# Optimization experiments

Hardware: AMD Instinct MI355X
Metric: run time of the kernel (lower is better)

## Reference

```python
import jax, jax.numpy as jnp
import numpy as np

PRED_LEN = 24
F, I, H = 64, 128, 512  # features_size, input_size, hidden_size
B, S = 1024, 168        # batch, seq_len


def setup_inputs() -> dict:
    key = jax.random.key(0)
    ks = jax.random.split(key, 14)
    s = 0.05
    return {
        "x": jax.random.normal(ks[0], (B, S, F), dtype=jnp.float32),
        "W_enc": jax.random.normal(ks[1], (I, F), dtype=jnp.float32) * s,
        "b_enc": jax.random.normal(ks[2], (I,), dtype=jnp.float32) * s,
        "Wih0": jax.random.normal(ks[3], (4 * H, I), dtype=jnp.float32) * s,
        "Whh0": jax.random.normal(ks[4], (4 * H, H), dtype=jnp.float32) * s,
        "bih0": jax.random.normal(ks[5], (4 * H,), dtype=jnp.float32) * s,
        "bhh0": jax.random.normal(ks[6], (4 * H,), dtype=jnp.float32) * s,
        "Wih1": jax.random.normal(ks[7], (4 * H, H), dtype=jnp.float32) * s,
        "Whh1": jax.random.normal(ks[8], (4 * H, H), dtype=jnp.float32) * s,
        "bih1": jax.random.normal(ks[9], (4 * H,), dtype=jnp.float32) * s,
        "bhh1": jax.random.normal(ks[10], (4 * H,), dtype=jnp.float32) * s,
        "W_dec": jax.random.normal(ks[11], (F, H), dtype=jnp.float32) * s,
        "b_dec": jax.random.normal(ks[12], (F,), dtype=jnp.float32) * s,
    }


def _lstm_cell(xt, h, c, Wih, Whh, bih, bhh):
    # PyTorch gate order: i, f, g, o
    gates = xt @ Wih.T + h @ Whh.T + (bih + bhh)
    i, f, g, o = jnp.split(gates, 4, axis=-1)
    c = jax.nn.sigmoid(f) * c + jax.nn.sigmoid(i) * jnp.tanh(g)
    h = jax.nn.sigmoid(o) * jnp.tanh(c)
    return h, c


def reference(x, W_enc, b_enc, Wih0, Whh0, bih0, bhh0,
              Wih1, Whh1, bih1, bhh1, W_dec, b_dec):
    batch = x.shape[0]
    h0 = jnp.zeros((batch, H), x.dtype)
    init = (h0, h0, h0, h0)  # (h_l0, c_l0, h_l1, c_l1)

    def step(carry, xt):
        hl0, cl0, hl1, cl1 = carry
        enc = xt @ W_enc.T + b_enc
        hl0, cl0 = _lstm_cell(enc, hl0, cl0, Wih0, Whh0, bih0, bhh0)
        hl1, cl1 = _lstm_cell(hl0, hl1, cl1, Wih1, Whh1, bih1, bhh1)
        out = hl1 @ W_dec.T + b_dec
        return (hl0, cl0, hl1, cl1), out

    # teacher-forced pass over the observed sequence; keep only last output
    carry, outs = jax.lax.scan(step, init, jnp.transpose(x, (1, 0, 2)))
    last = outs[-1]  # [B, F], prediction for step seq_len (idx = seq_len-1)

    def ar_step(state, _):
        carry, prev = state
        carry, out = step(carry, prev)
        return (carry, out), out

    _, ar_outs = jax.lax.scan(ar_step, (carry, last), None, length=PRED_LEN - 1)
    outputs = jnp.concatenate([last[None], ar_outs], axis=0)  # [pred_len, B, F]
    return jnp.transpose(outputs, (1, 0, 2))  # [B, pred_len, F]
```

## Files before the change

### kernel.cpp

```cpp
#include <hip/hip_runtime.h>

#define B_   1024
#define S_   168
#define F_   64
#define I_   128
#define H_   512
#define G4   2048
#define PRED 24

typedef unsigned short u16;
typedef unsigned int   u32;
typedef __attribute__((ext_vector_type(8))) __bf16 bf16x8;
typedef __attribute__((ext_vector_type(4))) float  f32x4;
typedef __attribute__((ext_vector_type(4))) int    i32x4;

__device__ __forceinline__ u16 f2bf(float f) {
  u32 u = __float_as_uint(f);
  u += 0x7fff + ((u >> 16) & 1);
  return (u16)(u >> 16);
}
__device__ __forceinline__ float bf2f(u16 h) {
  return __uint_as_float(((u32)h) << 16);
}
__device__ __forceinline__ float sigm(float x) {
  x = fminf(fmaxf(x, -30.f), 30.f);
  return 1.f / (1.f + __expf(-x));
}
__device__ __forceinline__ float tanh_(float x) {
  x = fminf(fmaxf(x, -15.f), 15.f);
  float e = __expf(2.f * x);
  return (e - 1.f) / (e + 1.f);
}


__global__ void k_split(const float* __restrict__ src, u16* __restrict__ hi,
                        u16* __restrict__ lo, int n) {
  for (int i = blockIdx.x * 256 + threadIdx.x; i < n; i += gridDim.x * 256) {
    float a = src[i];
    u16 h = f2bf(a);
    hi[i] = h;
    lo[i] = f2bf(a - bf2f(h));
  }
}

__global__ void k_w0c(const float* __restrict__ Wih0, const float* __restrict__ Wenc,
                      float* __restrict__ W0c) {
  int id = blockIdx.x * 256 + threadIdx.x;
  int j = id >> 6, f = id & 63;
  float s = 0.f;
  for (int i = 0; i < 128; ++i) s += Wih0[j * 128 + i] * Wenc[i * 64 + f];
  W0c[id] = s;
}

__global__ void k_w0cd(const float* __restrict__ W0c, const float* __restrict__ Wdec,
                       float* __restrict__ W0cd) {
  int id = blockIdx.x * 256 + threadIdx.x;
  int j = id >> 9, m = id & 511;
  float s = 0.f;
  for (int f = 0; f < 64; ++f) s += W0c[j * 64 + f] * Wdec[f * 512 + m];
  W0cd[id] = s;
}

__global__ void k_biases(const float* __restrict__ Wih0, const float* __restrict__ benc,
                         const float* __restrict__ bih0, const float* __restrict__ bhh0,
                         const float* __restrict__ bih1, const float* __restrict__ bhh1,
                         float* __restrict__ b0c, float* __restrict__ b1c) {
  int j = blockIdx.x * 256 + threadIdx.x;
  float s = 0.f;
  for (int i = 0; i < 128; ++i) s += Wih0[j * 128 + i] * benc[i];
  b0c[j] = s + bih0[j] + bhh0[j];
  b1c[j] = bih1[j] + bhh1[j];
}

__global__ void k_b0ar(const float* __restrict__ W0c, const float* __restrict__ bdec,
                       const float* __restrict__ b0c, float* __restrict__ b0ar) {
  int j = blockIdx.x * 256 + threadIdx.x;
  float s = 0.f;
  for (int f = 0; f < 64; ++f) s += W0c[j * 64 + f] * bdec[f];
  b0ar[j] = b0c[j] + s;
}

__global__ void k_pack(const float* __restrict__ W, int K, u16* __restrict__ dst) {
  int id = blockIdx.x * 256 + threadIdx.x;
  int lane = id & 63, fi = id >> 6;
  int NK = K >> 5;
  int kt = fi % NK, jg = fi / NK;
  int g = jg & 3, jt = jg >> 2;
  int j = jt * 16 + (lane & 15);
  int kb = kt * 32 + (lane >> 4) * 8;
  const float* src = W + (size_t)(g * 512 + j) * K + kb;
  u16 hi[8] __attribute__((aligned(16)));
  u16 lo[8] __attribute__((aligned(16)));
#pragma unroll
  for (int e = 0; e < 8; ++e) {
    float v = src[e];
    u16 h = f2bf(v);
    hi[e] = h;
    lo[e] = f2bf(v - bf2f(h));
  }
  u16* d = dst + (size_t)fi * 1024 + lane * 8;
  *(i32x4*)d = *(const i32x4*)hi;
  *(i32x4*)(d + 512) = *(const i32x4*)lo;
}


struct CellArgs {
  const u16* A1hi; const u16* A1lo; int strideA1; int K1;
  const u16* W1p;
  const u16* A2hi; const u16* A2lo;
  const u16* W2p;
  const float* bias;
  float* c;
  u16* hhi; u16* hlo;
};

struct DecArgs {
  const u16* hhi; const u16* hlo;
  const float* Wdec; const float* bdec;
  float* out;
};

__device__ __forceinline__ void cell_body(const CellArgs& P, u16* smem_,
                                          int t, int jblk, int mblk) {
  const u16* __restrict__ A1hi = P.A1hi;
  const u16* __restrict__ A1lo = P.A1lo;
  const int strideA1 = P.strideA1;
  const int K1 = P.K1;
  const u16* __restrict__ W1p = P.W1p;
  const u16* __restrict__ A2hi = P.A2hi;
  const u16* __restrict__ A2lo = P.A2lo;
  const u16* __restrict__ W2p = P.W2p;
  const float* __restrict__ bias = P.bias;
  float* __restrict__ c = P.c;
  u16* __restrict__ hhi = P.hhi;
  u16* __restrict__ hlo = P.hlo;

  const int mbase = mblk * 64;
  const int lane = t & 63, wv = t >> 6;
  const int mi = wv >> 1, jh = wv & 1;
  const int lr = lane & 15, qk = lane >> 4;
  const int jtg = jblk * 2 + jh;
  const int nc1 = (K1 == 64) ? 1 : 4;
  const int NC  = nc1 + 4;
  const int NK1 = K1 >> 5;

  f32x4 acc[4];
#pragma unroll
  for (int g = 0; g < 4; ++g) acc[g] = (f32x4){0.f, 0.f, 0.f, 0.f};

  auto prm = [&](int cc, const u16*& Ah, const u16*& Al, int& st, int& kb, int& Kc,
                 const u16*& Wp, int& NK) {
    if (cc < nc1) { Ah = A1hi; Al = A1lo; st = strideA1; kb = cc * 128;
                    Kc = (K1 == 64) ? 64 : 128; Wp = W1p; NK = NK1; }
    else { int i = cc - nc1; Ah = A2hi; Al = A2lo; st = 512; kb = i * 128;
           Kc = 128; Wp = W2p; NK = 16; }
  };

  auto stageLoad = [&](int cc, i32x4* rr) {
    const u16 *Ah, *Al, *Wp_; int st, kb, Kc, NK;
    prm(cc, Ah, Al, st, kb, Kc, Wp_, NK);
    const int ppr = Kc >> 3;
    const int npc = (Kc == 128) ? 4 : 2;
#pragma unroll 4
    for (int p = 0; p < npc; ++p) {
      int li   = p * 512 + t;
      int part = li >= 64 * ppr;
      int liw  = li - part * 64 * ppr;
      int rown = (ppr == 16) ? (liw >> 4) : (liw >> 3);
      int kp   = liw & (ppr - 1);
      const u16* src = (part ? Al : Ah) + (size_t)(mbase + rown) * st + kb + kp * 8;
      rr[p] = *(const i32x4*)src;
    }
  };
  auto stageWrite = [&](int cc, const i32x4* rr, int buf) {
    const int Kc  = (cc < nc1 && K1 == 64) ? 64 : 128;
    const int ppr = Kc >> 3;
    const int npc = (Kc == 128) ? 4 : 2;
    u16* sb = smem_ + buf * 16384;
#pragma unroll 4
    for (int p = 0; p < npc; ++p) {
      int li   = p * 512 + t;
      int part = li >= 64 * ppr;
      int liw  = li - part * 64 * ppr;
      int rown = (ppr == 16) ? (liw >> 4) : (liw >> 3);
      int kp   = liw & (ppr - 1);
      *(i32x4*)&sb[(((part * 64 + rown) * ppr) + (kp ^ (rown & (ppr - 1)))) * 8] = rr[p];
    }
  };
  auto loadW = [&](const u16* Wp_, int NK, int kt, i32x4* wh, i32x4* wl) {
#pragma unroll
    for (int g = 0; g < 4; ++g) {
      const u16* p = Wp_ + (size_t)((jtg * 4 + g) * NK + kt) * 1024 + lane * 8;
      wh[g] = *(const i32x4*)p;
      wl[g] = *(const i32x4*)(p + 512);
    }
  };
  auto mstep = [&](int buf, int ppr, const u16* Wp_, int NK, int kb5) {
    const u16* sb = smem_ + buf * 16384;
    const int nkt  = ppr >> 2;
    const int rowA = mi * 16 + lr;
    const int rmask = rowA & (ppr - 1);
#pragma unroll 4
    for (int kt = 0; kt < nkt; ++kt) {
      i32x4 wh[4], wl[4];
      loadW(Wp_, NK, kb5 + kt, wh, wl);
      int pl = (kt * 4 + qk) ^ rmask;
      bf16x8 ah = *(const bf16x8*)&sb[(rowA * ppr + pl) * 8];
      bf16x8 al = *(const bf16x8*)&sb[((64 + rowA) * ppr + pl) * 8];
#pragma unroll
      for (int g = 0; g < 4; ++g) {
        bf16x8 bh = __builtin_bit_cast(bf16x8, wh[g]);
        bf16x8 bl = __builtin_bit_cast(bf16x8, wl[g]);
        acc[g] = __builtin_amdgcn_mfma_f32_16x16x32_bf16(ah, bh, acc[g], 0, 0, 0);
        acc[g] = __builtin_amdgcn_mfma_f32_16x16x32_bf16(al, bh, acc[g], 0, 0, 0);
        acc[g] = __builtin_amdgcn_mfma_f32_16x16x32_bf16(ah, bl, acc[g], 0, 0, 0);
      }
    }
  };

  i32x4 sreg[4];

  stageLoad(0, sreg);
  stageWrite(0, sreg, 0);
  __syncthreads();

  for (int cc = 0; cc < NC; ++cc) {
    const int buf  = cc & 1;
    const bool more = (cc + 1 < NC);
    if (more) stageLoad(cc + 1, sreg);
    {
      const u16 *Ah, *Al, *Wp_; int st, kb, Kc, NK;
      prm(cc, Ah, Al, st, kb, Kc, Wp_, NK);
      mstep(buf, Kc >> 3, Wp_, NK, kb >> 5);
    }
    if (more) stageWrite(cc + 1, sreg, buf ^ 1);
    __syncthreads();
  }

  const int   j   = jblk * 32 + jh * 16 + lr;
  const float bi  = bias[j];
  const float bff = bias[512 + j];
  const float bg  = bias[1024 + j];
  const float bo  = bias[1536 + j];
#pragma unroll
  for (int rr = 0; rr < 4; ++rr) {
    int b   = mbase + mi * 16 + qk * 4 + rr;
    int idx = b * 512 + j;
    float iv = sigm(acc[0][rr] + bi);
    float fv = sigm(acc[1][rr] + bff);
    float gv = tanh_(acc[2][rr] + bg);
    float ov = sigm(acc[3][rr] + bo);
    float cn = fv * c[idx] + iv * gv;
    c[idx] = cn;
    float hn = ov * tanh_(cn);
    u16 hh = f2bf(hn);
    hhi[idx] = hh;
    hlo[idx] = f2bf(hn - bf2f(hh));
  }
}

__device__ __forceinline__ void dec_body(const DecArgs& D, float* smemf,
                                         int t, int bx, int by) {
  if (by >= 8) return;
  float (*sH)[65] = (float (*)[65])smemf;
  const int bbase = bx * 64;
  const int mbase = by * 64;
  {
    int b  = bbase + (t >> 3);
    int m0 = (t & 7) * 8;
    i32x4 hv = *(const i32x4*)&D.hhi[(size_t)b * 512 + mbase + m0];
    i32x4 lv = *(const i32x4*)&D.hlo[(size_t)b * 512 + mbase + m0];
    const u16* hp = (const u16*)&hv;
    const u16* lp = (const u16*)&lv;
#pragma unroll
    for (int e = 0; e < 8; ++e)
      sH[t >> 3][m0 + e] = bf2f(hp[e]) + bf2f(lp[e]);
  }
  __syncthreads();
  const int bl = t & 63;
  const int wv = t >> 6;
  float acc[8];
#pragma unroll
  for (int u = 0; u < 8; ++u) acc[u] = 0.f;
  for (int m = 0; m < 64; ++m) {
    float hv = sH[bl][m];
#pragma unroll
    for (int u = 0; u < 8; ++u)
      acc[u] += hv * D.Wdec[(size_t)(u * 8 + wv) * 512 + mbase + m];
  }
#pragma unroll
  for (int u = 0; u < 8; ++u) {
    int f = u * 8 + wv;
    float v = acc[u];
    if (by == 0) v += D.bdec[f];
    atomicAdd(&D.out[(size_t)(bbase + bl) * (PRED * F_) + f], v);
  }
}


__global__ __launch_bounds__(512, 4) void lstm3(CellArgs a) {
  __shared__ __align__(16) u16 smem_[32768];
  cell_body(a, smem_, threadIdx.x, blockIdx.x, blockIdx.y);
}

__global__ __launch_bounds__(512, 4) void lstm3_dual(CellArgs a0, CellArgs a1) {
  __shared__ __align__(16) u16 smem_[32768];
  if (blockIdx.z == 0) cell_body(a0, smem_, threadIdx.x, blockIdx.x, blockIdx.y);
  else                 cell_body(a1, smem_, threadIdx.x, blockIdx.x, blockIdx.y);
}

__global__ __launch_bounds__(512, 4) void lstm3_cell_dec(CellArgs a, DecArgs d) {
  __shared__ __align__(16) u16 smem_[32768];
  if (blockIdx.z == 0) cell_body(a, smem_, threadIdx.x, blockIdx.x, blockIdx.y);
  else                 dec_body(d, (float*)smem_, threadIdx.x, blockIdx.x, blockIdx.y);
}

__global__ __launch_bounds__(512) void k_decoder2(DecArgs d) {
  __shared__ __align__(16) float sm[64 * 65];
  dec_body(d, sm, threadIdx.x, blockIdx.x, blockIdx.y);
}


extern "C" void kernel_launch(void* const* d_in, const int* in_sizes, int n_in,
                              void* d_out, int out_size, void* d_ws, size_t ws_size,
                              hipStream_t stream) {
  const float* x    = (const float*)d_in[0];
  const float* Wenc = (const float*)d_in[1];
  const float* benc = (const float*)d_in[2];
  const float* Wih0 = (const float*)d_in[3];
  const float* Whh0 = (const float*)d_in[4];
  const float* bih0 = (const float*)d_in[5];
  const float* bhh0 = (const float*)d_in[6];
  const float* Wih1 = (const float*)d_in[7];
  const float* Whh1 = (const float*)d_in[8];
  const float* bih1 = (const float*)d_in[9];
  const float* bhh1 = (const float*)d_in[10];
  const float* Wdec = (const float*)d_in[11];
  const float* bdec = (const float*)d_in[12];
  float* out = (float*)d_out;

  char* p = (char*)d_ws;
  auto carve = [&](size_t bytes) { char* r = p; p += (bytes + 255) & ~(size_t)255; return r; };
  const size_t NX = (size_t)B_ * S_ * F_;
  const size_t NH = (size_t)B_ * H_;
  const size_t WP512 = (size_t)G4 * 512 * 2;
  u16* Xhi    = (u16*)carve(NX * 2);
  u16* Xlo    = (u16*)carve(NX * 2);
  float* W0c  = (float*)carve((size_t)G4 * 64 * 4);
  float* W0cd = (float*)carve((size_t)G4 * 512 * 4);
  u16* W0cp   = (u16*)carve((size_t)G4 * 64 * 2 * 2);
  u16* W0cdp  = (u16*)carve(WP512 * 2);
  u16* Whh0p  = (u16*)carve(WP512 * 2);
  u16* Wih1p  = (u16*)carve(WP512 * 2);
  u16* Whh1p  = (u16*)carve(WP512 * 2);
  float* b0c  = (float*)carve(G4 * 4);
  float* b0ar = (float*)carve(G4 * 4);
  float* b1c  = (float*)carve(G4 * 4);
  u16* h0hi[2] = {(u16*)carve(NH * 2), (u16*)carve(NH * 2)};
  u16* h0lo[2] = {(u16*)carve(NH * 2), (u16*)carve(NH * 2)};
  u16* h1hi[2] = {(u16*)carve(NH * 2), (u16*)carve(NH * 2)};
  u16* h1lo[2] = {(u16*)carve(NH * 2), (u16*)carve(NH * 2)};
  float* c0 = (float*)carve(NH * 4);
  float* c1 = (float*)carve(NH * 4);
  (void)ws_size; (void)n_in; (void)in_sizes;

  hipMemsetAsync(d_out, 0, (size_t)out_size * 4, stream);
  hipMemsetAsync(h0hi[0], 0, NH * 2, stream);
  hipMemsetAsync(h0lo[0], 0, NH * 2, stream);
  hipMemsetAsync(h1hi[0], 0, NH * 2, stream);
  hipMemsetAsync(h1lo[0], 0, NH * 2, stream);
  hipMemsetAsync(c0, 0, NH * 4, stream);
  hipMemsetAsync(c1, 0, NH * 4, stream);

  k_split<<<4096, 256, 0, stream>>>(x, Xhi, Xlo, (int)NX);
  k_w0c<<<512, 256, 0, stream>>>(Wih0, Wenc, W0c);
  k_w0cd<<<4096, 256, 0, stream>>>(W0c, Wdec, W0cd);
  k_biases<<<8, 256, 0, stream>>>(Wih0, benc, bih0, bhh0, bih1, bhh1, b0c, b1c);
  k_b0ar<<<8, 256, 0, stream>>>(W0c, bdec, b0c, b0ar);
  k_pack<<<32 * 16, 256, 0, stream>>>(Whh0, 512, Whh0p);
  k_pack<<<32 * 16, 256, 0, stream>>>(Wih1, 512, Wih1p);
  k_pack<<<32 * 16, 256, 0, stream>>>(Whh1, 512, Whh1p);
  k_pack<<<32 * 16, 256, 0, stream>>>(W0cd, 512, W0cdp);
  k_pack<<<32 * 2, 256, 0, stream>>>(W0c, 64, W0cp);

  dim3 grid(16, 16);
  dim3 grid2(16, 16, 2);

  {
    CellArgs l0 = {Xhi, Xlo, S_ * F_, 64, W0cp,
                   h0hi[0], h0lo[0], Whh0p, b0c, c0, h0hi[1], h0lo[1]};
    lstm3<<<grid, 512, 0, stream>>>(l0);
  }
  for (int s = 0; s < S_ - 1; ++s) {
    int pp = s & 1, np = 1 - pp;
    CellArgs l1 = {h0hi[np], h0lo[np], 512, 512, Wih1p,
                   h1hi[pp], h1lo[pp], Whh1p, b1c, c1, h1hi[np], h1lo[np]};
    CellArgs l0 = {Xhi + (size_t)(s + 1) * F_, Xlo + (size_t)(s + 1) * F_, S_ * F_, 64, W0cp,
                   h0hi[np], h0lo[np], Whh0p, b0c, c0, h0hi[pp], h0lo[pp]};
    lstm3_dual<<<grid2, 512, 0, stream>>>(l1, l0);
  }
  {
    CellArgs l1 = {h0hi[0], h0lo[0], 512, 512, Wih1p,
                   h1hi[1], h1lo[1], Whh1p, b1c, c1, h1hi[0], h1lo[0]};
    lstm3<<<grid, 512, 0, stream>>>(l1);
  }

  for (int s = S_ - 1; s < S_ + PRED - 1; ++s) {
    int pp = s & 1, np = 1 - pp;
    DecArgs d = {h1hi[np], h1lo[np], Wdec, bdec, out + (size_t)(s - (S_ - 1)) * F_};
    if (s + 1 < S_ + PRED - 1) {
      CellArgs l0 = {h1hi[np], h1lo[np], 512, 512, W0cdp,
                     h0hi[np], h0lo[np], Whh0p, b0ar, c0, h0hi[pp], h0lo[pp]};
      lstm3_cell_dec<<<grid2, 512, 0, stream>>>(l0, d);
      CellArgs l1 = {h0hi[pp], h0lo[pp], 512, 512, Wih1p,
                     h1hi[np], h1lo[np], Whh1p, b1c, c1, h1hi[pp], h1lo[pp]};
      lstm3<<<grid, 512, 0, stream>>>(l1);
    } else {
      k_decoder2<<<dim3(16, 8), 512, 0, stream>>>(d);
    }
  }
}
```

Baseline: 8.297 ms.

## Software-pipeline weight fragment loads and remap cell block indices for L2 locality

```diff
diff --git a/kernel.cpp b/kernel.cpp
--- a/kernel.cpp
+++ b/kernel.cpp
@@ -103,6 +103,9 @@
   *(i32x4*)(d + 512) = *(const i32x4*)lo;
 }
 
+
+struct PPR16 { static constexpr int v = 16; };
+struct PPR8  { static constexpr int v = 8;  };
 
 struct CellArgs {
   const u16* A1hi; const u16* A1lo; int strideA1; int K1;
@@ -195,31 +198,47 @@
       wl[g] = *(const i32x4*)(p + 512);
     }
   };
-  auto mstep = [&](int buf, int ppr, const u16* Wp_, int NK, int kb5) {
+
+  i32x4 whA[4], wlA[4];
+
+  auto mstep = [&](auto PPRt, int buf, const u16* WpC, int NKC, int kb5C,
+                   const u16* WpN, int NKN, int kb5N, bool haveNext) {
+    constexpr int ppr = decltype(PPRt)::v;
+    constexpr int nkt = ppr >> 2;
     const u16* sb = smem_ + buf * 16384;
-    const int nkt  = ppr >> 2;
     const int rowA = mi * 16 + lr;
     const int rmask = rowA & (ppr - 1);
-#pragma unroll 4
+#pragma unroll
     for (int kt = 0; kt < nkt; ++kt) {
-      i32x4 wh[4], wl[4];
-      loadW(Wp_, NK, kb5 + kt, wh, wl);
+      i32x4 whN[4], wlN[4];
+      const bool pf = (kt + 1 < nkt) || haveNext;
+      if (kt + 1 < nkt)      loadW(WpC, NKC, kb5C + kt + 1, whN, wlN);
+      else if (haveNext)     loadW(WpN, NKN, kb5N, whN, wlN);
       int pl = (kt * 4 + qk) ^ rmask;
       bf16x8 ah = *(const bf16x8*)&sb[(rowA * ppr + pl) * 8];
       bf16x8 al = *(const bf16x8*)&sb[((64 + rowA) * ppr + pl) * 8];
 #pragma unroll
       for (int g = 0; g < 4; ++g) {
-        bf16x8 bh = __builtin_bit_cast(bf16x8, wh[g]);
-        bf16x8 bl = __builtin_bit_cast(bf16x8, wl[g]);
+        bf16x8 bh = __builtin_bit_cast(bf16x8, whA[g]);
+        bf16x8 bl = __builtin_bit_cast(bf16x8, wlA[g]);
         acc[g] = __builtin_amdgcn_mfma_f32_16x16x32_bf16(ah, bh, acc[g], 0, 0, 0);
         acc[g] = __builtin_amdgcn_mfma_f32_16x16x32_bf16(al, bh, acc[g], 0, 0, 0);
         acc[g] = __builtin_amdgcn_mfma_f32_16x16x32_bf16(ah, bl, acc[g], 0, 0, 0);
       }
+      if (pf) {
+#pragma unroll
+        for (int g = 0; g < 4; ++g) { whA[g] = whN[g]; wlA[g] = wlN[g]; }
+      }
     }
   };
 
   i32x4 sreg[4];
 
+  {
+    const u16 *Ah, *Al, *Wp_; int st, kb, Kc, NK;
+    prm(0, Ah, Al, st, kb, Kc, Wp_, NK);
+    loadW(Wp_, NK, kb >> 5, whA, wlA);
+  }
   stageLoad(0, sreg);
   stageWrite(0, sreg, 0);
   __syncthreads();
@@ -228,11 +247,12 @@
     const int buf  = cc & 1;
     const bool more = (cc + 1 < NC);
     if (more) stageLoad(cc + 1, sreg);
-    {
-      const u16 *Ah, *Al, *Wp_; int st, kb, Kc, NK;
-      prm(cc, Ah, Al, st, kb, Kc, Wp_, NK);
-      mstep(buf, Kc >> 3, Wp_, NK, kb >> 5);
-    }
+    const u16 *Ah, *Al, *WpC; int st, kb, Kc, NKC;
+    prm(cc, Ah, Al, st, kb, Kc, WpC, NKC);
+    const u16 *Ah2, *Al2, *WpN = 0; int st2, kb2 = 0, Kc2, NKN = 0;
+    if (more) prm(cc + 1, Ah2, Al2, st2, kb2, Kc2, WpN, NKN);
+    if (Kc == 128) mstep(PPR16{}, buf, WpC, NKC, kb >> 5, WpN, NKN, kb2 >> 5, more);
+    else           mstep(PPR8{},  buf, WpC, NKC, kb >> 5, WpN, NKN, kb2 >> 5, more);
     if (more) stageWrite(cc + 1, sreg, buf ^ 1);
     __syncthreads();
   }
@@ -259,6 +279,12 @@
   }
 }
 
+__device__ __forceinline__ void cell_remap(int bx, int by, int& jblk, int& mblk) {
+  int bid = by * 16 + bx;
+  jblk = (bid & 7) + ((bid >> 7) << 3);
+  mblk = (bid >> 3) & 15;
+}
+
 __device__ __forceinline__ void dec_body(const DecArgs& D, float* smemf,
                                          int t, int bx, int by) {
   if (by >= 8) return;
@@ -300,19 +326,25 @@
 
 __global__ __launch_bounds__(512, 4) void lstm3(CellArgs a) {
   __shared__ __align__(16) u16 smem_[32768];
-  cell_body(a, smem_, threadIdx.x, blockIdx.x, blockIdx.y);
+  int jb, mb; cell_remap(blockIdx.x, blockIdx.y, jb, mb);
+  cell_body(a, smem_, threadIdx.x, jb, mb);
 }
 
 __global__ __launch_bounds__(512, 4) void lstm3_dual(CellArgs a0, CellArgs a1) {
   __shared__ __align__(16) u16 smem_[32768];
-  if (blockIdx.z == 0) cell_body(a0, smem_, threadIdx.x, blockIdx.x, blockIdx.y);
-  else                 cell_body(a1, smem_, threadIdx.x, blockIdx.x, blockIdx.y);
+  int jb, mb; cell_remap(blockIdx.x, blockIdx.y, jb, mb);
+  if (blockIdx.z == 0) cell_body(a0, smem_, threadIdx.x, jb, mb);
+  else                 cell_body(a1, smem_, threadIdx.x, jb, mb);
 }
 
 __global__ __launch_bounds__(512, 4) void lstm3_cell_dec(CellArgs a, DecArgs d) {
   __shared__ __align__(16) u16 smem_[32768];
-  if (blockIdx.z == 0) cell_body(a, smem_, threadIdx.x, blockIdx.x, blockIdx.y);
-  else                 dec_body(d, (float*)smem_, threadIdx.x, blockIdx.x, blockIdx.y);
+  if (blockIdx.z == 0) {
+    int jb, mb; cell_remap(blockIdx.x, blockIdx.y, jb, mb);
+    cell_body(a, smem_, threadIdx.x, jb, mb);
+  } else {
+    dec_body(d, (float*)smem_, threadIdx.x, blockIdx.x, blockIdx.y);
+  }
 }
 
 __global__ __launch_bounds__(512) void k_decoder2(DecArgs d) {
```

New measurement: 16.18 ms. 94.9% more time.
